# Performance work log

Hardware: AMD Instinct MI355X
Metric: run time of the kernel (lower is better)

Reference implementation:

```python
import jax, jax.numpy as jnp
import numpy as np

N_NODES = 100000
N_EDGES = 1600000
D = 128


def setup_inputs() -> dict:
    key = jax.random.key(0)
    ks = jax.random.split(key, 10)
    s = 1.0 / np.sqrt(D)
    return {
        "feat": jax.random.normal(ks[0], (N_NODES, D), dtype=jnp.float32),
        "W_self0": jax.random.normal(ks[1], (D, D), dtype=jnp.float32) * s,
        "W_neigh0": jax.random.normal(ks[2], (D, D), dtype=jnp.float32) * s,
        "b0": jnp.zeros((D,), dtype=jnp.float32),
        "W_self1": jax.random.normal(ks[3], (D, D), dtype=jnp.float32) * s,
        "W_neigh1": jax.random.normal(ks[4], (D, D), dtype=jnp.float32) * s,
        "b1": jnp.zeros((D,), dtype=jnp.float32),
        "ln_g": jnp.ones((D,), dtype=jnp.float32),
        "ln_b": jnp.zeros((D,), dtype=jnp.float32),
        "edge_src": jax.random.randint(ks[5], (N_EDGES,), 0, N_NODES, dtype=jnp.int32),
        "edge_dst": jax.random.randint(ks[6], (N_EDGES,), 0, N_NODES, dtype=jnp.int32),
        "in_deg": jax.random.randint(ks[7], (N_NODES,), 1, 64, dtype=jnp.int32),
    }


def _sage_layer(h, src, dst, inv_deg, W_self, W_neigh, b):
    # mean aggregation over incoming neighbors: gather -> segment_sum -> scale
    msg = jax.ops.segment_sum(h[src], dst, num_segments=N_NODES)  # [N, d]
    h_neigh = msg * inv_deg[:, None]
    return h @ W_self + h_neigh @ W_neigh + b


def _layer_norm(x, g, b, eps=1e-5):
    mu = jnp.mean(x, axis=-1, keepdims=True)
    var = jnp.mean((x - mu) ** 2, axis=-1, keepdims=True)
    return (x - mu) * jax.lax.rsqrt(var + eps) * g + b


def reference(feat, W_self0, W_neigh0, b0, W_self1, W_neigh1, b1, ln_g, ln_b,
              edge_src, edge_dst, in_deg):
    # Eval mode: dropout = identity, no EmbeddingSelector / reg loss.
    inv_deg = 1.0 / jnp.maximum(in_deg, 1).astype(feat.dtype)
    h = _sage_layer(feat, edge_src, edge_dst, inv_deg, W_self0, W_neigh0, b0)
    h = _layer_norm(h, ln_g, ln_b)
    h = jax.nn.relu(h)
    h = _sage_layer(h, edge_src, edge_dst, inv_deg, W_self1, W_neigh1, b1)
    return h
```

## Files before the change

### kernel.cpp

```cpp
#include <hip/hip_runtime.h>

#define D 128
#define NN 100000
#define PB 391
#define EPB 4096
#define PREP_BLKS 12756

typedef __attribute__((ext_vector_type(8))) short short8;
typedef __attribute__((ext_vector_type(16))) float floatx16;
typedef __attribute__((ext_vector_type(2))) float floatx2;

__device__ inline unsigned short bf16_rne(float f) {
    unsigned int u = __float_as_uint(f);
    u += 0x7fff + ((u >> 16) & 1);
    return (unsigned short)(u >> 16);
}
__device__ inline unsigned char fp8_enc1(float f) {
    return (unsigned char)(__builtin_amdgcn_cvt_pk_fp8_f32(f, f, 0, false) & 0xff);
}

__global__ __launch_bounds__(256) void prep_count_kernel(
    const float* __restrict__ feat, unsigned short* __restrict__ feat16,
    unsigned char* __restrict__ feat8,
    const float* __restrict__ Ws0, const float* __restrict__ Wn0,
    const float* __restrict__ Ws1, const float* __restrict__ Wn1,
    unsigned short* __restrict__ wt0, unsigned short* __restrict__ wt1,
    const int* __restrict__ dst, unsigned int* __restrict__ bucketCnt,
    unsigned int* __restrict__ blockBase, int E)
{
    __shared__ unsigned int h[PB];
    int bid = blockIdx.x;
    if (bid < 12500) {
        int i = bid * 256 + threadIdx.x;
        float4 v = *(const float4*)(feat + (size_t)i * 4);
        unsigned short u[4] = { bf16_rne(v.x), bf16_rne(v.y), bf16_rne(v.z), bf16_rne(v.w) };
        *(uint2*)(feat16 + (size_t)i * 4) = *(uint2*)u;
        int w = __builtin_amdgcn_cvt_pk_fp8_f32(v.x, v.y, 0, false);
        w = __builtin_amdgcn_cvt_pk_fp8_f32(v.z, v.w, w, true);
        ((unsigned int*)feat8)[i] = (unsigned int)w;
    } else if (bid < PREP_BLKS) {
        int i = (bid - 12500) * 256 + threadIdx.x;
        int layer = i >> 15;
        int r = i & 32767;
        int n = r >> 8;
        int k = r & 255;
        const float* Ws = layer ? Ws1 : Ws0;
        const float* Wn = layer ? Wn1 : Wn0;
        float v = (k < 128) ? Ws[(size_t)k * 128 + n] : Wn[(size_t)(k - 128) * 128 + n];
        unsigned short* wt = layer ? wt1 : wt0;
        int ct = n >> 5, nn = n & 31;
        int hs = k >> 7, k7 = k & 127;
        int kc = k7 >> 4, hf = (k7 >> 3) & 1, j = k7 & 7;
        int frag = ((((ct * 2 + hs) * 8 + kc) * 2 + hf) * 32 + nn) * 8 + j;
        wt[frag] = bf16_rne(v);
    } else {
        const int b = bid - PREP_BLKS;
        const int t = threadIdx.x;
        for (int i = t; i < PB; i += 256) h[i] = 0;
        __syncthreads();
        const int base = b * EPB;
#pragma unroll
        for (int k = 0; k < EPB / 256; k++) {
            int e = base + k * 256 + t;
            if (e < E) atomicAdd(&h[(unsigned)dst[e] >> 8], 1u);
        }
        __syncthreads();
        for (int i = t; i < PB; i += 256) {
            unsigned int c = h[i];
            unsigned int o = 0;
            if (c) o = atomicAdd(&bucketCnt[i], c);
            blockBase[(size_t)b * PB + i] = o;
        }
    }
}

__global__ __launch_bounds__(512) void part_scan_kernel(
    const unsigned int* __restrict__ bucketCnt, unsigned int* __restrict__ bucketStart,
    int E)
{
    __shared__ unsigned int sd[512];
    int t = threadIdx.x;
    unsigned int v = (t < PB) ? bucketCnt[t] : 0u;
    sd[t] = v; __syncthreads();
    for (int off = 1; off < 512; off <<= 1) {
        unsigned int x = (t >= off) ? sd[t - off] : 0u;
        __syncthreads();
        sd[t] += x;
        __syncthreads();
    }
    if (t < PB) bucketStart[t] = sd[t] - v;
    if (t == 0) bucketStart[PB] = (unsigned int)E;
}

__global__ __launch_bounds__(256) void part_scatter_kernel(
    const int* __restrict__ src, const int* __restrict__ dst,
    const unsigned int* __restrict__ bucketStart,
    const unsigned int* __restrict__ blockBase,
    unsigned int* __restrict__ pairs, int E)
{
    __shared__ unsigned int h[PB];
    const int t = threadIdx.x;
    const int b = blockIdx.x;
    for (int i = t; i < PB; i += 256) h[i] = 0;
    __syncthreads();
    const int base = b * EPB;
#pragma unroll
    for (int k = 0; k < EPB / 256; k++) {
        int e = base + k * 256 + t;
        if (e < E) {
            unsigned int d = (unsigned int)dst[e];
            unsigned int bk = d >> 8;
            unsigned int lr = atomicAdd(&h[bk], 1u);
            unsigned int pos = bucketStart[bk] + blockBase[(size_t)b * PB + bk] + lr;
            pairs[pos] = ((unsigned int)src[e] << 8) | (d & 255u);
        }
    }
}

__global__ __launch_bounds__(256) void part_fine_kernel(
    const unsigned int* __restrict__ pairs, const unsigned int* __restrict__ bucketStart,
    int* __restrict__ row_ptr, int* __restrict__ col, int N, int E)
{
    __shared__ unsigned int h[256], sc[256], pos[256];
    const int t = threadIdx.x;
    const int b = blockIdx.x;
    h[t] = 0;
    __syncthreads();
    const unsigned int ebeg = bucketStart[b];
    const unsigned int eend = bucketStart[b + 1];
    for (unsigned int i = ebeg + t; i < eend; i += 256)
        atomicAdd(&h[pairs[i] & 255u], 1u);
    __syncthreads();
    sc[t] = h[t]; __syncthreads();
    for (int off = 1; off < 256; off <<= 1) {
        unsigned int x = (t >= off) ? sc[t - off] : 0u;
        __syncthreads();
        sc[t] += x;
        __syncthreads();
    }
    unsigned int excl = sc[t] - h[t];
    int node = b * 256 + t;
    if (node < N) row_ptr[node] = (int)(ebeg + excl);
    pos[t] = ebeg + excl;
    if (b == 0 && t == 0) row_ptr[N] = E;
    __syncthreads();
    for (unsigned int i = ebeg + t; i < eend; i += 256) {
        unsigned int p = pairs[i];
        unsigned int w = atomicAdd(&pos[p & 255u], 1u);
        col[w] = (int)(p >> 8);
    }
}

__global__ __launch_bounds__(256) void gather8_kernel(
    const unsigned char* __restrict__ h8, const int* __restrict__ row_ptr,
    const int* __restrict__ col, const int* __restrict__ in_deg,
    unsigned short* __restrict__ msg16, int N)
{
    const int wave = threadIdx.x >> 6;
    const int lane = threadIdx.x & 63;
    const int quad = lane >> 4;
    const int ln16 = lane & 15;
    const int node = (blockIdx.x * 4 + wave) * 4 + quad;
    if (node >= N) return;

    const size_t lo = (size_t)ln16 * 8;
    int beg = row_ptr[node];
    int end = row_ptr[node + 1];

    float f[8] = {0.f,0.f,0.f,0.f,0.f,0.f,0.f,0.f};
    int j = beg;
    for (; j + 4 <= end; j += 4) {
        int c0 = col[j], c1 = col[j + 1], c2 = col[j + 2], c3 = col[j + 3];
        uint2 u0 = *(const uint2*)(h8 + (size_t)c0 * D + lo);
        uint2 u1 = *(const uint2*)(h8 + (size_t)c1 * D + lo);
        uint2 u2 = *(const uint2*)(h8 + (size_t)c2 * D + lo);
        uint2 u3 = *(const uint2*)(h8 + (size_t)c3 * D + lo);
#pragma unroll
        for (int q = 0; q < 4; q++) {
            uint2 u = q == 0 ? u0 : q == 1 ? u1 : q == 2 ? u2 : u3;
            floatx2 p0 = __builtin_amdgcn_cvt_pk_f32_fp8((int)u.x, false);
            floatx2 p1 = __builtin_amdgcn_cvt_pk_f32_fp8((int)u.x, true);
            floatx2 p2 = __builtin_amdgcn_cvt_pk_f32_fp8((int)u.y, false);
            floatx2 p3 = __builtin_amdgcn_cvt_pk_f32_fp8((int)u.y, true);
            f[0] += p0.x; f[1] += p0.y; f[2] += p1.x; f[3] += p1.y;
            f[4] += p2.x; f[5] += p2.y; f[6] += p3.x; f[7] += p3.y;
        }
    }
    for (; j < end; ++j) {
        uint2 u = *(const uint2*)(h8 + (size_t)col[j] * D + lo);
        floatx2 p0 = __builtin_amdgcn_cvt_pk_f32_fp8((int)u.x, false);
        floatx2 p1 = __builtin_amdgcn_cvt_pk_f32_fp8((int)u.x, true);
        floatx2 p2 = __builtin_amdgcn_cvt_pk_f32_fp8((int)u.y, false);
        floatx2 p3 = __builtin_amdgcn_cvt_pk_f32_fp8((int)u.y, true);
        f[0] += p0.x; f[1] += p0.y; f[2] += p1.x; f[3] += p1.y;
        f[4] += p2.x; f[5] += p2.y; f[6] += p3.x; f[7] += p3.y;
    }
    int dg = in_deg[node];
    float invd = 1.f / (float)(dg > 1 ? dg : 1);
    unsigned short us[8];
#pragma unroll
    for (int i = 0; i < 8; i++) us[i] = bf16_rne(f[i] * invd);
    *(uint4*)(msg16 + (size_t)node * D + ln16 * 8) = *(const uint4*)us;
}

__global__ __launch_bounds__(256, 4) void mfma32_kernel(
    const unsigned short* __restrict__ A16, const unsigned short* __restrict__ Msg16,
    const unsigned short* __restrict__ Wt,
    const float* __restrict__ bias,
    const float* __restrict__ ln_g, const float* __restrict__ ln_b,
    unsigned short* __restrict__ Out16, unsigned char* __restrict__ Out8,
    float* __restrict__ Out32, int N, int do_ln)
{
    const int tid  = threadIdx.x;
    const int wave = tid >> 6;
    const int lane = tid & 63;
    const int half = lane >> 5;
    const int n32  = lane & 31;
    const int brow0 = blockIdx.x * 128;
    const int wrow0 = brow0 + wave * 32;

    const int arow = wrow0 + n32;
    const bool arv = arow < N;
    const size_t koff = (size_t)half * 8;

    floatx16 acc[4];
#pragma unroll
    for (int ct = 0; ct < 4; ct++)
#pragma unroll
        for (int r = 0; r < 16; r++) acc[ct][r] = 0.f;

#pragma unroll
    for (int hs = 0; hs < 2; hs++) {
        const unsigned short* Asrc = hs ? Msg16 : A16;
#pragma unroll
        for (int kc = 0; kc < 8; kc++) {
            short8 a;
            if (arv) a = *(const short8*)(Asrc + (size_t)arow * D + kc * 16 + koff);
            else     a = (short8){0,0,0,0,0,0,0,0};
#pragma unroll
            for (int ct = 0; ct < 4; ct++) {
                short8 b = *(const short8*)(Wt + ((size_t)((ct * 2 + hs) * 8 + kc) * 64 + lane) * 8);
                acc[ct] = __builtin_amdgcn_mfma_f32_32x32x16_bf16(a, b, acc[ct], 0, 0, 0);
            }
        }
    }

#pragma unroll
    for (int ct = 0; ct < 4; ct++) {
        float bb = bias[ct * 32 + n32];
#pragma unroll
        for (int r = 0; r < 16; r++) acc[ct][r] += bb;
    }

    if (do_ln) {
        float gg[4], be[4];
#pragma unroll
        for (int ct = 0; ct < 4; ct++) {
            gg[ct] = ln_g[ct * 32 + n32];
            be[ct] = ln_b[ct * 32 + n32];
        }
        float s[16], s2[16];
#pragma unroll
        for (int r = 0; r < 16; r++) {
            s[r]  = acc[0][r] + acc[1][r] + acc[2][r] + acc[3][r];
            s2[r] = acc[0][r]*acc[0][r] + acc[1][r]*acc[1][r]
                  + acc[2][r]*acc[2][r] + acc[3][r]*acc[3][r];
        }
#pragma unroll
        for (int off = 1; off < 32; off <<= 1) {
#pragma unroll
            for (int r = 0; r < 16; r++) {
                s[r]  += __shfl_xor(s[r],  off);
                s2[r] += __shfl_xor(s2[r], off);
            }
        }
#pragma unroll
        for (int r = 0; r < 16; r++) {
            float mean = s[r] * (1.f / 128.f);
            float var  = s2[r] * (1.f / 128.f) - mean * mean;
            float rstd = rsqrtf(var + 1e-5f);
            int row = wrow0 + (r & 3) + 8 * (r >> 2) + 4 * half;
            if (row < N) {
#pragma unroll
                for (int ct = 0; ct < 4; ct++) {
                    float t = (acc[ct][r] - mean) * rstd * gg[ct] + be[ct];
                    t = t > 0.f ? t : 0.f;
                    Out16[(size_t)row * D + ct * 32 + n32] = bf16_rne(t);
                    Out8 [(size_t)row * D + ct * 32 + n32] = fp8_enc1(t);
                }
            }
        }
    } else {
#pragma unroll
        for (int r = 0; r < 16; r++) {
            int row = wrow0 + (r & 3) + 8 * (r >> 2) + 4 * half;
            if (row < N) {
#pragma unroll
                for (int ct = 0; ct < 4; ct++)
                    Out32[(size_t)row * D + ct * 32 + n32] = acc[ct][r];
            }
        }
    }
}

extern "C" void kernel_launch(void* const* d_in, const int* in_sizes, int n_in,
                              void* d_out, int out_size, void* d_ws, size_t ws_size,
                              hipStream_t stream)
{
    const float* feat = (const float*)d_in[0];
    const float* Ws0  = (const float*)d_in[1];
    const float* Wn0  = (const float*)d_in[2];
    const float* b0   = (const float*)d_in[3];
    const float* Ws1  = (const float*)d_in[4];
    const float* Wn1  = (const float*)d_in[5];
    const float* b1   = (const float*)d_in[6];
    const float* lng  = (const float*)d_in[7];
    const float* lnb  = (const float*)d_in[8];
    const int* esrc   = (const int*)d_in[9];
    const int* edst   = (const int*)d_in[10];
    const int* indeg  = (const int*)d_in[11];

    const int N = NN;
    const int E = in_sizes[9];

    float* out = (float*)d_out;

    const int nblk = (E + EPB - 1) / EPB;
    char* ws = (char*)d_ws;
    size_t o = 0;
    auto alloc = [&](size_t bytes) { char* p = ws + o; o += (bytes + 15) & ~(size_t)15; return p; };
    unsigned short* feat16 = (unsigned short*)alloc((size_t)N * D * 2);
    int* col     = (int*)alloc((size_t)E * 4);
    int* row_ptr = (int*)alloc((size_t)(N + 1) * 4);
    unsigned short* wt0 = (unsigned short*)alloc(128 * 256 * 2);
    unsigned short* wt1 = (unsigned short*)alloc(128 * 256 * 2);
    size_t csr_bytes = (size_t)(512 + 512 + (size_t)nblk * PB + E) * 4 + 64;
    char* regD = alloc((size_t)N * D * 2 > csr_bytes ? (size_t)N * D * 2 : csr_bytes);
    unsigned int* bucketCnt   = (unsigned int*)regD;
    unsigned int* bucketStart = bucketCnt + 512;
    unsigned int* blockBase   = bucketStart + 512;
    unsigned int* pairs       = blockBase + (size_t)nblk * PB;
    unsigned short* h116 = (unsigned short*)regD;

    unsigned short* msg0  = (unsigned short*)d_out;
    unsigned char*  feat8 = (unsigned char*)d_out + (size_t)N * D * 2;
    unsigned char*  h18   = (unsigned char*)d_out + (size_t)N * D * 3;
    unsigned short* msg1  = feat16;
    (void)ws_size;

    const int gemm_blocks = (N + 127) / 128;
    const int gather_blocks = (N + 15) / 16;

    hipMemsetAsync(bucketCnt, 0, 512 * 4, stream);
    prep_count_kernel<<<PREP_BLKS + nblk, 256, 0, stream>>>(
        feat, feat16, feat8, Ws0, Wn0, Ws1, Wn1, wt0, wt1,
        edst, bucketCnt, blockBase, E);

    part_scan_kernel<<<1, 512, 0, stream>>>(bucketCnt, bucketStart, E);
    part_scatter_kernel<<<nblk, 256, 0, stream>>>(esrc, edst, bucketStart, blockBase, pairs, E);
    part_fine_kernel<<<PB, 256, 0, stream>>>(pairs, bucketStart, row_ptr, col, N, E);

    gather8_kernel<<<gather_blocks, 256, 0, stream>>>(feat8, row_ptr, col, indeg, msg0, N);
    mfma32_kernel<<<gemm_blocks, 256, 0, stream>>>(
        feat16, msg0, wt0, b0, lng, lnb, h116, h18, nullptr, N, 1);

    gather8_kernel<<<gather_blocks, 256, 0, stream>>>(h18, row_ptr, col, indeg, msg1, N);
    mfma32_kernel<<<gemm_blocks, 256, 0, stream>>>(
        h116, msg1, wt1, b1, nullptr, nullptr, nullptr, nullptr, out, N, 0);
}
```

Baseline: 345.2 us.

## Store bf16 activations in MFMA fragment layout and stage LN outputs through LDS

The bf16 feature and message buffers are now written in a tiled MFMA-fragment order, so the GEMM kernel loads each A fragment as one contiguous short8 per lane instead of strided row loads. The layer-norm epilogue writes bf16 and fp8 results into swizzled shared memory, then emits coalesced 16-byte global stores, replacing the scattered 2-byte and 1-byte stores. Occupancy bound drops from 4 to 3 blocks to accommodate 48KB of LDS. Risks: the tail tile is clamped when N is not a multiple of 32, and the gather kernel must read the new layout consistently.

```diff
diff --git a/kernel.cpp b/kernel.cpp
--- a/kernel.cpp
+++ b/kernel.cpp
@@ -18,6 +18,7 @@
 __device__ inline unsigned char fp8_enc1(float f) {
     return (unsigned char)(__builtin_amdgcn_cvt_pk_fp8_f32(f, f, 0, false) & 0xff);
 }
+
 
 __global__ __launch_bounds__(256) void prep_count_kernel(
     const float* __restrict__ feat, unsigned short* __restrict__ feat16,
@@ -34,7 +35,10 @@
         int i = bid * 256 + threadIdx.x;
         float4 v = *(const float4*)(feat + (size_t)i * 4);
         unsigned short u[4] = { bf16_rne(v.x), bf16_rne(v.y), bf16_rne(v.z), bf16_rne(v.w) };
-        *(uint2*)(feat16 + (size_t)i * 4) = *(uint2*)u;
+        int n  = i >> 5;
+        int d0 = (i & 31) * 4;
+        size_t f = (size_t)(n >> 5) * 4096 + (size_t)((d0 >> 3) * 32 + (n & 31)) * 8 + (d0 & 7);
+        *(uint2*)(feat16 + f) = *(uint2*)u;
         int w = __builtin_amdgcn_cvt_pk_fp8_f32(v.x, v.y, 0, false);
         w = __builtin_amdgcn_cvt_pk_fp8_f32(v.z, v.w, w, true);
         ((unsigned int*)feat8)[i] = (unsigned int)w;
@@ -200,10 +204,11 @@
     unsigned short us[8];
 #pragma unroll
     for (int i = 0; i < 8; i++) us[i] = bf16_rne(f[i] * invd);
-    *(uint4*)(msg16 + (size_t)node * D + ln16 * 8) = *(const uint4*)us;
-}
-
-__global__ __launch_bounds__(256, 4) void mfma32_kernel(
+    size_t fo = (size_t)(node >> 5) * 4096 + ((size_t)ln16 * 32 + (node & 31)) * 8;
+    *(uint4*)(msg16 + fo) = *(const uint4*)us;
+}
+
+__global__ __launch_bounds__(256, 3) void mfma32_kernel(
     const unsigned short* __restrict__ A16, const unsigned short* __restrict__ Msg16,
     const unsigned short* __restrict__ Wt,
     const float* __restrict__ bias,
@@ -211,6 +216,8 @@
     unsigned short* __restrict__ Out16, unsigned char* __restrict__ Out8,
     float* __restrict__ Out32, int N, int do_ln)
 {
+    __shared__ char smem[49152];
+
     const int tid  = threadIdx.x;
     const int wave = tid >> 6;
     const int lane = tid & 63;
@@ -219,9 +226,11 @@
     const int brow0 = blockIdx.x * 128;
     const int wrow0 = brow0 + wave * 32;
 
-    const int arow = wrow0 + n32;
-    const bool arv = arow < N;
-    const size_t koff = (size_t)half * 8;
+    const int NT = N >> 5;
+    int tile = wrow0 >> 5;
+    if (tile >= NT) tile = NT - 1;
+    const short8* Af = (const short8*)(A16   + (size_t)tile * 4096);
+    const short8* Mf = (const short8*)(Msg16 + (size_t)tile * 4096);
 
     floatx16 acc[4];
 #pragma unroll
@@ -231,12 +240,10 @@
 
 #pragma unroll
     for (int hs = 0; hs < 2; hs++) {
-        const unsigned short* Asrc = hs ? Msg16 : A16;
+        const short8* Sf = hs ? Mf : Af;
 #pragma unroll
         for (int kc = 0; kc < 8; kc++) {
-            short8 a;
-            if (arv) a = *(const short8*)(Asrc + (size_t)arow * D + kc * 16 + koff);
-            else     a = (short8){0,0,0,0,0,0,0,0};
+            short8 a = Sf[kc * 64 + lane];
 #pragma unroll
             for (int ct = 0; ct < 4; ct++) {
                 short8 b = *(const short8*)(Wt + ((size_t)((ct * 2 + hs) * 8 + kc) * 64 + lane) * 8);
@@ -245,12 +252,15 @@
         }
     }
 
-#pragma unroll
-    for (int ct = 0; ct < 4; ct++) {
-        float bb = bias[ct * 32 + n32];
-#pragma unroll
-        for (int r = 0; r < 16; r++) acc[ct][r] += bb;
-    }
+    float bb[4];
+#pragma unroll
+    for (int ct = 0; ct < 4; ct++) bb[ct] = bias[ct * 32 + n32];
+
+    float v[4][16];
+#pragma unroll
+    for (int ct = 0; ct < 4; ct++)
+#pragma unroll
+        for (int r = 0; r < 16; r++) v[ct][r] = acc[ct][r] + bb[ct];
 
     if (do_ln) {
         float gg[4], be[4];
@@ -262,9 +272,8 @@
         float s[16], s2[16];
 #pragma unroll
         for (int r = 0; r < 16; r++) {
-            s[r]  = acc[0][r] + acc[1][r] + acc[2][r] + acc[3][r];
-            s2[r] = acc[0][r]*acc[0][r] + acc[1][r]*acc[1][r]
-                  + acc[2][r]*acc[2][r] + acc[3][r]*acc[3][r];
+            s[r]  = v[0][r] + v[1][r] + v[2][r] + v[3][r];
+            s2[r] = v[0][r]*v[0][r] + v[1][r]*v[1][r] + v[2][r]*v[2][r] + v[3][r]*v[3][r];
         }
 #pragma unroll
         for (int off = 1; off < 32; off <<= 1) {
@@ -274,21 +283,36 @@
                 s2[r] += __shfl_xor(s2[r], off);
             }
         }
+        unsigned char* sO8 = (unsigned char*)smem + 32768;
 #pragma unroll
         for (int r = 0; r < 16; r++) {
             float mean = s[r] * (1.f / 128.f);
             float var  = s2[r] * (1.f / 128.f) - mean * mean;
             float rstd = rsqrtf(var + 1e-5f);
-            int row = wrow0 + (r & 3) + 8 * (r >> 2) + 4 * half;
-            if (row < N) {
-#pragma unroll
-                for (int ct = 0; ct < 4; ct++) {
-                    float t = (acc[ct][r] - mean) * rstd * gg[ct] + be[ct];
-                    t = t > 0.f ? t : 0.f;
-                    Out16[(size_t)row * D + ct * 32 + n32] = bf16_rne(t);
-                    Out8 [(size_t)row * D + ct * 32 + n32] = fp8_enc1(t);
-                }
+            int brow = wave * 32 + (r & 3) + 8 * (r >> 2) + 4 * half;
+#pragma unroll
+            for (int ct = 0; ct < 4; ct++) {
+                float t = (v[ct][r] - mean) * rstd * gg[ct] + be[ct];
+                t = t > 0.f ? t : 0.f;
+                int slot = (ct * 4 + (n32 >> 3)) ^ (brow & 15);
+                *(unsigned short*)(smem + brow * 256 + slot * 16 + (n32 & 7) * 2) = bf16_rne(t);
+                sO8[brow * 128 + ct * 32 + n32] = fp8_enc1(t);
             }
+        }
+        __syncthreads();
+#pragma unroll
+        for (int i = 0; i < 8; i++) {
+            int ch = tid + i * 256;
+            int tl = ch >> 9, p = ch & 511, kc2 = p >> 5, rr = p & 31;
+            if (brow0 + tl * 32 + rr < N)
+                *(uint4*)(Out16 + (size_t)brow0 * D + ch * 8) =
+                    *(const uint4*)&smem[(tl * 32 + rr) * 256 + ((kc2 ^ (rr & 15)) * 16)];
+        }
+#pragma unroll
+        for (int i = 0; i < 4; i++) {
+            int ch = tid + i * 256;
+            if (brow0 + (ch >> 3) < N)
+                *(uint4*)(Out8 + (size_t)brow0 * D + ch * 16) = *(const uint4*)&sO8[ch * 16];
         }
     } else {
 #pragma unroll
@@ -297,7 +321,7 @@
             if (row < N) {
 #pragma unroll
                 for (int ct = 0; ct < 4; ct++)
-                    Out32[(size_t)row * D + ct * 32 + n32] = acc[ct][r];
+                    Out32[(size_t)row * D + ct * 32 + n32] = v[ct][r];
             }
         }
     }
```

Result: faster. 308.8 us (-10.5%).
